# Kernel optimization log

Measured on AMD Instinct MI355X. Metric: run time of the kernel, lower is better.

## Reference

```python
import jax, jax.numpy as jnp
import numpy as np

N = 4096        # num gaussians
H = 128         # image height
W = 128         # image width
ZOOM = 0.5
EPS = 1e-6


def _normalize(q):
    # torch F.normalize(dim=1): q / max(||q||, 1e-12)
    n = jnp.linalg.norm(q, axis=1, keepdims=True)
    return q / jnp.maximum(n, 1e-12)


def _left_quat_matrix(q):
    # q: (N,4) = (w,x,y,z); left-multiplication matrix L(q) so that q*p = L(q) p
    w, x, y, z = q[:, 0], q[:, 1], q[:, 2], q[:, 3]
    return jnp.stack([
        jnp.stack([w, -x, -y, -z], -1),
        jnp.stack([x,  w, -z,  y], -1),
        jnp.stack([y,  z,  w, -x], -1),
        jnp.stack([z, -y,  x,  w], -1)], axis=1)


def _right_quat_matrix_conj(q):
    # right-multiplication matrix of conj(q): R(conj(q)) = R(q)^T
    w, x, y, z = q[:, 0], q[:, 1], q[:, 2], q[:, 3]
    return jnp.stack([
        jnp.stack([ w,  x,  y,  z], -1),
        jnp.stack([-x,  w,  z, -y], -1),
        jnp.stack([-y, -z,  w,  x], -1),
        jnp.stack([-z,  y, -x,  w], -1)], axis=1)


def setup_inputs() -> dict:
    key = jax.random.key(0)
    k1, k2, k3, k4, k5 = jax.random.split(key, 5)
    means = jax.random.normal(k1, (N, 4), dtype=jnp.float32)
    raw_scales = jax.random.normal(k2, (N, 4), dtype=jnp.float32)
    rotors = jax.random.normal(k3, (N, 8), dtype=jnp.float32)
    t = jax.random.uniform(k4, (), dtype=jnp.float32)
    angle = jax.random.uniform(k5, (), dtype=jnp.float32)
    return {"means": means, "raw_scales": raw_scales, "rotors": rotors,
            "t": t, "angle": angle}


def reference(means, raw_scales, rotors, t, angle):
    scale = jnp.exp(raw_scales)                              # (N,4)
    sign = jnp.array([1.0, -1.0, -1.0, -1.0], jnp.float32)
    q1 = _normalize(rotors[:, jnp.array([0, 4, 5, 6])])
    q2 = _normalize(rotors[:, jnp.array([7, 1, 2, 3])] * sign)
    L = _left_quat_matrix(q1)                                # (N,4,4)
    Rm = _right_quat_matrix_conj(q2)                         # (N,4,4)
    R4 = jnp.einsum('nij,njk->nik', L, Rm)                   # (N,4,4)
    # cov4D = R4 diag(scale^2) R4^T
    cov4D = jnp.einsum('nij,nj,nkj->nik', R4, scale * scale, R4)

    U = cov4D[:, :3, :3]                                     # (N,3,3)
    V = cov4D[:, :3, 3]                                      # (N,3)
    Wm = jnp.maximum(cov4D[:, 3, 3], EPS)                    # (N,)
    lambda_t = 1.0 / Wm

    mu_xyz = means[:, :3]
    mu_t = means[:, 3]
    time_diff = t - mu_t                                     # (N,)
    mu3D = mu_xyz + V * (time_diff / Wm)[:, None]            # (N,3)

    sin_a, cos_a = jnp.sin(angle), jnp.cos(angle)
    z0, o1 = jnp.zeros(()), jnp.ones(())
    view = jnp.stack([jnp.stack([cos_a, z0, sin_a]),
                      jnp.stack([z0, o1, z0]),
                      jnp.stack([-sin_a, z0, cos_a])])       # (3,3)

    mu3D_view = mu3D @ view.T                                # (N,3)
    cov3D = U - jnp.einsum('ni,nj->nij', V, V) / Wm[:, None, None]
    cov3D_view = jnp.einsum('ij,njk,lk->nil', view, cov3D, view)

    scale_mat = jnp.array([[(W - 1) / 2 * ZOOM, 0.0, 0.0],
                           [0.0, (H - 1) / 2 * ZOOM, 0.0]], jnp.float32)
    offset = jnp.array([(W - 1) / 2, (H - 1) / 2], jnp.float32)
    mu2D = mu3D_view @ scale_mat.T + offset                  # (N,2)
    cov2D = jnp.einsum('ij,njk,lk->nil', scale_mat, cov3D_view, scale_mat)
    cov2D = cov2D + jnp.eye(2, dtype=jnp.float32) * EPS      # (N,2,2)

    # analytic 2x2 inverse (same as torch.linalg.inv for 2x2)
    a, b = cov2D[:, 0, 0], cov2D[:, 0, 1]
    c, d = cov2D[:, 1, 0], cov2D[:, 1, 1]
    det = a * d - b * c
    inv_cov2D = jnp.stack([jnp.stack([d, -b], -1),
                           jnp.stack([-c, a], -1)], axis=1) / det[:, None, None]

    weights = jnp.exp(-0.5 * lambda_t * time_diff ** 2)      # (N,)

    yy, xx = jnp.meshgrid(jnp.arange(H, dtype=jnp.float32),
                          jnp.arange(W, dtype=jnp.float32), indexing='ij')
    grid = jnp.stack([xx, yy], -1).reshape(-1, 2)            # (P,2), P=H*W

    delta = grid[None, :, :] - mu2D[:, None, :]              # (N,P,2)
    expo = -0.5 * jnp.einsum('npi,nij,npj->np', delta, inv_cov2D, delta)
    patch = weights[:, None] * jnp.exp(expo)                 # (N,P)
    image = patch.sum(axis=0).reshape(H, W)
    image = image / jnp.maximum(image.max(), EPS)
    return image
```

## Files before the change

kernel.cpp:

```cpp
#include <hip/hip_runtime.h>
#include <math.h>

#define NG   4096
#define HH   128
#define WW   128
#define NPIX (HH*WW)
#define EPSF 1e-6f
#define CHUNK 128
#define NCH  (NG/CHUNK)
#define PXB  (NPIX/256)

#if __has_builtin(__builtin_amdgcn_exp2f)
#define EXP2F(x) __builtin_amdgcn_exp2f(x)
#else
#define EXP2F(x) exp2f(x)
#endif

__global__ __launch_bounds__(256) void prep_kernel(
    const float* __restrict__ means, const float* __restrict__ raw_scales,
    const float* __restrict__ rotors, const float* __restrict__ tp,
    const float* __restrict__ ap, float* __restrict__ params)
{
    int i = blockIdx.x * 256 + threadIdx.x;
    if (i >= NG) return;
    float t = tp[0], angle = ap[0];

    float r0 = rotors[i*8+0], r1 = rotors[i*8+1], r2 = rotors[i*8+2], r3 = rotors[i*8+3];
    float r4 = rotors[i*8+4], r5 = rotors[i*8+5], r6 = rotors[i*8+6], r7 = rotors[i*8+7];

    float w1 = r0, x1 = r4, y1 = r5, z1 = r6;
    float n1 = sqrtf(w1*w1 + x1*x1 + y1*y1 + z1*z1);
    n1 = fmaxf(n1, 1e-12f);
    w1 /= n1; x1 /= n1; y1 /= n1; z1 /= n1;
    float w2 = r7, x2 = -r1, y2 = -r2, z2 = -r3;
    float n2 = sqrtf(w2*w2 + x2*x2 + y2*y2 + z2*z2);
    n2 = fmaxf(n2, 1e-12f);
    w2 /= n2; x2 /= n2; y2 /= n2; z2 /= n2;

    float L[4][4]  = {{w1,-x1,-y1,-z1},{x1,w1,-z1,y1},{y1,z1,w1,-x1},{z1,-y1,x1,w1}};
    float Rm[4][4] = {{w2, x2, y2, z2},{-x2,w2,z2,-y2},{-y2,-z2,w2,x2},{-z2,y2,-x2,w2}};

    float R4[4][4];
    #pragma unroll
    for (int a = 0; a < 4; ++a)
        #pragma unroll
        for (int b = 0; b < 4; ++b)
            R4[a][b] = L[a][0]*Rm[0][b] + L[a][1]*Rm[1][b] + L[a][2]*Rm[2][b] + L[a][3]*Rm[3][b];

    float s2[4];
    #pragma unroll
    for (int j = 0; j < 4; ++j) {
        float e = expf(raw_scales[i*4+j]);
        s2[j] = e * e;
    }

    float cov[4][4];
    #pragma unroll
    for (int a = 0; a < 4; ++a)
        #pragma unroll
        for (int b = a; b < 4; ++b) {
            float s = R4[a][0]*s2[0]*R4[b][0] + R4[a][1]*s2[1]*R4[b][1]
                    + R4[a][2]*s2[2]*R4[b][2] + R4[a][3]*s2[3]*R4[b][3];
            cov[a][b] = s; cov[b][a] = s;
        }

    float Wm   = fmaxf(cov[3][3], EPSF);
    float invW = 1.0f / Wm;
    float V0 = cov[0][3], V1 = cov[1][3], V2 = cov[2][3];
    float td = t - means[i*4+3];

    float mu0 = means[i*4+0] + V0 * td * invW;
    float mu1 = means[i*4+1] + V1 * td * invW;
    float mu2 = means[i*4+2] + V2 * td * invW;

    float ca = cosf(angle), sa = sinf(angle);
    float mvx = ca*mu0 + sa*mu2;
    float mvy = mu1;

    float C00 = cov[0][0] - V0*V0*invW;
    float C01 = cov[0][1] - V0*V1*invW;
    float C02 = cov[0][2] - V0*V2*invW;
    float C11 = cov[1][1] - V1*V1*invW;
    float C12 = cov[1][2] - V1*V2*invW;
    float C22 = cov[2][2] - V2*V2*invW;

    float cv00 = ca*ca*C00 + 2.f*ca*sa*C02 + sa*sa*C22;
    float cv01 = ca*C01 + sa*C12;
    float cv11 = C11;

    const float Ksc = 31.75f;
    const float K2  = Ksc * Ksc;
    float a = K2*cv00 + EPSF;
    float b = K2*cv01;
    float d = K2*cv11 + EPSF;
    float det = a*d - b*b;
    float invdet = 1.0f / det;

    const float L2E = 1.4426950408889634f;
    float A  = -0.5f * d * invdet * L2E;
    float B  =         b * invdet * L2E;
    float C  = -0.5f * a * invdet * L2E;
    float c0 = -0.5f * invW * td * td * L2E;

    float mux = Ksc*mvx + 63.5f;
    float muy = Ksc*mvy + 63.5f;

    float* p = params + i*8;
    p[0] = mux; p[1] = muy; p[2] = A; p[3] = B; p[4] = C; p[5] = c0;
    p[6] = 0.f; p[7] = 0.f;
}

__global__ __launch_bounds__(256) void accum_kernel(
    const float* __restrict__ params, float* __restrict__ acc)
{
    __shared__ float sp[CHUNK][8];
    int tid = threadIdx.x;
    int pb  = blockIdx.x & (PXB-1);
    int ch  = blockIdx.x / PXB;

    ((float4*)&sp[0][0])[tid] = ((const float4*)(params + ch*CHUNK*8))[tid];
    __syncthreads();

    int p = pb*256 + tid;
    float px = (float)(p & (WW-1));
    float py = (float)(p >> 7);

    float accv = 0.f;
    #pragma unroll 4
    for (int g = 0; g < CHUNK; ++g) {
        float4 v0 = *(const float4*)&sp[g][0];
        float2 v1 = *(const float2*)&sp[g][4];
        float dx = px - v0.x;
        float dy = py - v0.y;
        float e = fmaf(v0.z*dx, dx, fmaf(v0.w*dx, dy, fmaf(v1.x*dy, dy, v1.y)));
        accv += EXP2F(e);
    }
    atomicAdd(&acc[p], accv);
}

__global__ __launch_bounds__(256) void blockmax_kernel(
    const float* __restrict__ acc, float* __restrict__ bmax)
{
    int p = blockIdx.x*256 + threadIdx.x;
    float v = acc[p];
    #pragma unroll
    for (int off = 32; off > 0; off >>= 1)
        v = fmaxf(v, __shfl_xor(v, off));
    __shared__ float sm[4];
    if ((threadIdx.x & 63) == 0) sm[threadIdx.x >> 6] = v;
    __syncthreads();
    if (threadIdx.x == 0)
        bmax[blockIdx.x] = fmaxf(fmaxf(sm[0], sm[1]), fmaxf(sm[2], sm[3]));
}

__global__ __launch_bounds__(256) void norm_kernel(
    const float* __restrict__ acc, const float* __restrict__ bmax,
    float* __restrict__ out)
{
    float m = 0.f;
    for (int i = 0; i < PXB; ++i) m = fmaxf(m, bmax[i]);
    m = fmaxf(m, EPSF);
    int p = blockIdx.x*256 + threadIdx.x;
    out[p] = acc[p] / m;
}

extern "C" void kernel_launch(void* const* d_in, const int* in_sizes, int n_in,
                              void* d_out, int out_size, void* d_ws, size_t ws_size,
                              hipStream_t stream) {
    const float* means      = (const float*)d_in[0];
    const float* raw_scales = (const float*)d_in[1];
    const float* rotors     = (const float*)d_in[2];
    const float* t          = (const float*)d_in[3];
    const float* angle      = (const float*)d_in[4];
    float* out = (float*)d_out;

    float* params = (float*)d_ws;
    float* acc    = params + NG*8;
    float* bmax   = acc + NPIX;

    hipMemsetAsync(acc, 0, NPIX*sizeof(float), stream);
    prep_kernel<<<NG/256, 256, 0, stream>>>(means, raw_scales, rotors, t, angle, params);
    accum_kernel<<<PXB*NCH, 256, 0, stream>>>(params, acc);
    blockmax_kernel<<<PXB, 256, 0, stream>>>(acc, bmax);
    norm_kernel<<<PXB, 256, 0, stream>>>(acc, bmax, out);
}
```

Before: 90.52 us.

## Compute four pixels per thread via finite differences and merge kernels

```diff
diff --git a/kernel.cpp b/kernel.cpp
--- a/kernel.cpp
+++ b/kernel.cpp
@@ -8,7 +8,8 @@
 #define EPSF 1e-6f
 #define CHUNK 128
 #define NCH  (NG/CHUNK)
-#define PXB  (NPIX/256)
+#define PXT  4
+#define PXB  (NPIX/(256*PXT))
 
 #if __has_builtin(__builtin_amdgcn_exp2f)
 #define EXP2F(x) __builtin_amdgcn_exp2f(x)
@@ -19,22 +20,24 @@
 __global__ __launch_bounds__(256) void prep_kernel(
     const float* __restrict__ means, const float* __restrict__ raw_scales,
     const float* __restrict__ rotors, const float* __restrict__ tp,
-    const float* __restrict__ ap, float* __restrict__ params)
+    const float* __restrict__ ap, float* __restrict__ params,
+    float* __restrict__ acc)
 {
     int i = blockIdx.x * 256 + threadIdx.x;
     if (i >= NG) return;
+
+    ((float4*)acc)[i] = make_float4(0.f, 0.f, 0.f, 0.f);
+
     float t = tp[0], angle = ap[0];
 
     float r0 = rotors[i*8+0], r1 = rotors[i*8+1], r2 = rotors[i*8+2], r3 = rotors[i*8+3];
     float r4 = rotors[i*8+4], r5 = rotors[i*8+5], r6 = rotors[i*8+6], r7 = rotors[i*8+7];
 
     float w1 = r0, x1 = r4, y1 = r5, z1 = r6;
-    float n1 = sqrtf(w1*w1 + x1*x1 + y1*y1 + z1*z1);
-    n1 = fmaxf(n1, 1e-12f);
+    float n1 = fmaxf(sqrtf(w1*w1 + x1*x1 + y1*y1 + z1*z1), 1e-12f);
     w1 /= n1; x1 /= n1; y1 /= n1; z1 /= n1;
     float w2 = r7, x2 = -r1, y2 = -r2, z2 = -r3;
-    float n2 = sqrtf(w2*w2 + x2*x2 + y2*y2 + z2*z2);
-    n2 = fmaxf(n2, 1e-12f);
+    float n2 = fmaxf(sqrtf(w2*w2 + x2*x2 + y2*y2 + z2*z2), 1e-12f);
     w2 /= n2; x2 /= n2; y2 /= n2; z2 /= n2;
 
     float L[4][4]  = {{w1,-x1,-y1,-z1},{x1,w1,-z1,y1},{y1,z1,w1,-x1},{z1,-y1,x1,w1}};
@@ -106,62 +109,66 @@
     float muy = Ksc*mvy + 63.5f;
 
     float* p = params + i*8;
-    p[0] = mux; p[1] = muy; p[2] = A; p[3] = B; p[4] = C; p[5] = c0;
-    p[6] = 0.f; p[7] = 0.f;
+    p[0] = mux; p[1] = muy; p[2] = A; p[3] = B;
+    p[4] = C;   p[5] = c0;  p[6] = A + A; p[7] = 0.f;
 }
 
 __global__ __launch_bounds__(256) void accum_kernel(
     const float* __restrict__ params, float* __restrict__ acc)
 {
-    __shared__ float sp[CHUNK][8];
+    __shared__ float sp[CHUNK*8];
     int tid = threadIdx.x;
-    int pb  = blockIdx.x & (PXB-1);
+    int pxb = blockIdx.x & (PXB-1);
     int ch  = blockIdx.x / PXB;
 
-    ((float4*)&sp[0][0])[tid] = ((const float4*)(params + ch*CHUNK*8))[tid];
+    ((float4*)sp)[tid] = ((const float4*)(params + ch*CHUNK*8))[tid];
     __syncthreads();
 
-    int p = pb*256 + tid;
-    float px = (float)(p & (WW-1));
-    float py = (float)(p >> 7);
+    float px = (float)((tid & 31) * PXT);
+    float py = (float)(pxb * 8 + (tid >> 5));
 
-    float accv = 0.f;
+    float a0 = 0.f, a1 = 0.f, a2 = 0.f, a3 = 0.f;
     #pragma unroll 4
     for (int g = 0; g < CHUNK; ++g) {
-        float4 v0 = *(const float4*)&sp[g][0];
-        float2 v1 = *(const float2*)&sp[g][4];
+        const float* q = sp + g*8;
+        float4 v0 = *(const float4*)(q);
+        float4 v1 = *(const float4*)(q + 4);
         float dx = px - v0.x;
         float dy = py - v0.y;
-        float e = fmaf(v0.z*dx, dx, fmaf(v0.w*dx, dy, fmaf(v1.x*dy, dy, v1.y)));
-        accv += EXP2F(e);
+        float b1 = v0.w * dy;
+        float tt = fmaf(v1.x * dy, dy, v1.y);
+        float e  = fmaf(fmaf(v0.z, dx, b1), dx, tt);
+        float dd = fmaf(v0.z, fmaf(2.f, dx, 1.f), b1);
+        a0 += EXP2F(e); e += dd; dd += v1.z;
+        a1 += EXP2F(e); e += dd; dd += v1.z;
+        a2 += EXP2F(e); e += dd;
+        a3 += EXP2F(e);
     }
-    atomicAdd(&acc[p], accv);
-}
 
-__global__ __launch_bounds__(256) void blockmax_kernel(
-    const float* __restrict__ acc, float* __restrict__ bmax)
-{
-    int p = blockIdx.x*256 + threadIdx.x;
-    float v = acc[p];
-    #pragma unroll
-    for (int off = 32; off > 0; off >>= 1)
-        v = fmaxf(v, __shfl_xor(v, off));
-    __shared__ float sm[4];
-    if ((threadIdx.x & 63) == 0) sm[threadIdx.x >> 6] = v;
-    __syncthreads();
-    if (threadIdx.x == 0)
-        bmax[blockIdx.x] = fmaxf(fmaxf(sm[0], sm[1]), fmaxf(sm[2], sm[3]));
+    float* ap = acc + pxb*1024 + (tid >> 5)*128 + (tid & 31)*PXT;
+    atomicAdd(ap+0, a0); atomicAdd(ap+1, a1);
+    atomicAdd(ap+2, a2); atomicAdd(ap+3, a3);
 }
 
 __global__ __launch_bounds__(256) void norm_kernel(
-    const float* __restrict__ acc, const float* __restrict__ bmax,
-    float* __restrict__ out)
+    const float* __restrict__ acc, float* __restrict__ out)
 {
+    int tid = threadIdx.x;
     float m = 0.f;
-    for (int i = 0; i < PXB; ++i) m = fmaxf(m, bmax[i]);
+    #pragma unroll 8
+    for (int i = 0; i < NPIX/256; ++i)
+        m = fmaxf(m, acc[i*256 + tid]);
+    #pragma unroll
+    for (int off = 32; off > 0; off >>= 1)
+        m = fmaxf(m, __shfl_xor(m, off));
+    __shared__ float sm[4];
+    if ((tid & 63) == 0) sm[tid >> 6] = m;
+    __syncthreads();
+    m = fmaxf(fmaxf(sm[0], sm[1]), fmaxf(sm[2], sm[3]));
     m = fmaxf(m, EPSF);
-    int p = blockIdx.x*256 + threadIdx.x;
-    out[p] = acc[p] / m;
+    float inv = 1.0f / m;
+    int p = blockIdx.x*256 + tid;
+    out[p] = acc[p] * inv;
 }
 
 extern "C" void kernel_launch(void* const* d_in, const int* in_sizes, int n_in,
@@ -176,11 +183,8 @@
 
     float* params = (float*)d_ws;
     float* acc    = params + NG*8;
-    float* bmax   = acc + NPIX;
 
-    hipMemsetAsync(acc, 0, NPIX*sizeof(float), stream);
-    prep_kernel<<<NG/256, 256, 0, stream>>>(means, raw_scales, rotors, t, angle, params);
+    prep_kernel<<<NG/256, 256, 0, stream>>>(means, raw_scales, rotors, t, angle, params, acc);
     accum_kernel<<<PXB*NCH, 256, 0, stream>>>(params, acc);
-    blockmax_kernel<<<PXB, 256, 0, stream>>>(acc, bmax);
-    norm_kernel<<<PXB, 256, 0, stream>>>(acc, bmax, out);
+    norm_kernel<<<NPIX/256, 256, 0, stream>>>(acc, out);
 }
```

Result: slower. 92.80 us (+2.5%).
